# Optimization experiments

Measured on AMD Instinct MI355X. Metric: run time of the kernel, lower is better.

The kernel has to match this reference:

```python
import jax, jax.numpy as jnp
import numpy as np

N_NODES = 50000
N_EDGES = 800000
IN_DIM = 256
HID_DIM = 256
OUT_DIM = 2


def setup_inputs() -> dict:
    key = jax.random.key(0)
    ks = jax.random.split(key, 8)
    x = jax.random.normal(ks[0], (N_NODES, IN_DIM), dtype=jnp.float32)
    edge_index = jax.random.randint(ks[1], (2, N_EDGES), 0, N_NODES, dtype=jnp.int64)
    # GCNConv weights (PyG: out = norm_agg(x @ W) + b), Glorot-ish scale
    W1 = jax.random.normal(ks[2], (IN_DIM, HID_DIM), dtype=jnp.float32) / np.sqrt(IN_DIM)
    b1 = jnp.zeros((HID_DIM,), dtype=jnp.float32)
    W2 = jax.random.normal(ks[3], (HID_DIM, HID_DIM), dtype=jnp.float32) / np.sqrt(HID_DIM)
    b2 = jnp.zeros((HID_DIM,), dtype=jnp.float32)
    Wfc = jax.random.normal(ks[4], (HID_DIM, OUT_DIM), dtype=jnp.float32) / np.sqrt(HID_DIM)
    bfc = jnp.zeros((OUT_DIM,), dtype=jnp.float32)
    return {"x": x, "edge_index": edge_index, "W1": W1, "b1": b1,
            "W2": W2, "b2": b2, "Wfc": Wfc, "bfc": bfc}


def _edge_norm(edge_index, n_nodes):
    # GCNConv: add self-loops, symmetric normalization D^-1/2 A_hat D^-1/2
    loop = jnp.arange(n_nodes, dtype=edge_index.dtype)
    src = jnp.concatenate([edge_index[0], loop])  # [E+N]
    dst = jnp.concatenate([edge_index[1], loop])  # [E+N]
    deg = jax.ops.segment_sum(jnp.ones_like(dst, dtype=jnp.float32), dst,
                              num_segments=n_nodes)
    dis = jnp.where(deg > 0, jax.lax.rsqrt(deg), 0.0)  # deg_inv_sqrt [N]
    norm = dis[src] * dis[dst]  # [E+N]
    return src, dst, norm


def _gcn_layer(x, W, b, src, dst, norm, n_nodes):
    h = x @ W  # [N, F_out]
    msg = h[src] * norm[:, None]  # gather + scale, [E+N, F_out]
    return jax.ops.segment_sum(msg, dst, num_segments=n_nodes) + b


def reference(x, edge_index, W1, b1, W2, b2, Wfc, bfc):
    n = x.shape[0]
    src, dst, norm = _edge_norm(edge_index, n)
    h = jax.nn.relu(_gcn_layer(x, W1, b1, src, dst, norm, n))
    # dropout is identity in eval mode
    h = jax.nn.relu(_gcn_layer(h, W2, b2, src, dst, norm, n))
    logits = h @ Wfc + bfc
    return jax.nn.log_softmax(logits, axis=1)
```

## Files before the change

### kernel.cpp

```cpp
#include <hip/hip_runtime.h>
#include <math.h>

#define N_NODES 50000
#define N_EDGES 800000
#define DIM 256
#define SCAN_BLOCKS ((N_NODES + 255) / 256)
#define NXBLK 12500
#define NDEGBLK ((N_EDGES + 255) / 256)

typedef short bf16x8 __attribute__((ext_vector_type(8)));
typedef float f32x4 __attribute__((ext_vector_type(4)));

__device__ __forceinline__ float bf2f(unsigned short u) {
    return __uint_as_float(((unsigned)u) << 16);
}
__device__ __forceinline__ unsigned short f2bf(float f) {
    unsigned u = __float_as_uint(f);
    return (unsigned short)((u + 0x7fffu + ((u >> 16) & 1u)) >> 16);
}

__global__ __launch_bounds__(256) void k_prep(const float* __restrict__ x,
                                              unsigned short* __restrict__ xb,
                                              const float* __restrict__ W1,
                                              unsigned short* __restrict__ W1t,
                                              const float* __restrict__ W2,
                                              unsigned short* __restrict__ W2t,
                                              const int* __restrict__ dst,
                                              int* __restrict__ ideg) {
    int bid = blockIdx.x;
    int tid = threadIdx.x;
    if (bid < NXBLK) {
        int i = bid * 256 + tid;
        float4 v = ((const float4*)x)[i];
        ((ushort4*)xb)[i] = make_ushort4(f2bf(v.x), f2bf(v.y), f2bf(v.z), f2bf(v.w));
    } else if (bid < NXBLK + 256) {
        int n = bid - NXBLK;
        W1t[n * 256 + tid] = f2bf(W1[tid * 256 + n]);
    } else if (bid < NXBLK + 512) {
        int n = bid - NXBLK - 256;
        W2t[n * 256 + tid] = f2bf(W2[tid * 256 + n]);
    } else {
        int e = (bid - NXBLK - 512) * 256 + tid;
        if (e < N_EDGES) atomicAdd(&ideg[dst[e]], 1);
    }
}


__global__ __launch_bounds__(256) void k_scan_block(const int* __restrict__ ideg,
                                                    int* __restrict__ rowptr,
                                                    int* __restrict__ blocksum) {
    __shared__ int s[256];
    int t = threadIdx.x;
    int i = blockIdx.x * 256 + t;
    int v = (i < N_NODES) ? ideg[i] : 0;
    s[t] = v;
    for (int off = 1; off < 256; off <<= 1) {
        __syncthreads();
        int add = (t >= off) ? s[t - off] : 0;
        __syncthreads();
        s[t] += add;
    }
    __syncthreads();
    if (i < N_NODES) rowptr[i] = s[t] - v;
    if (t == 255) blocksum[blockIdx.x] = s[255];
}

__global__ __launch_bounds__(256) void k_scan_add(int* __restrict__ rowptr,
                                                  const int* __restrict__ blocksum,
                                                  int* __restrict__ cursor,
                                                  const int* __restrict__ ideg,
                                                  float* __restrict__ dis) {
    __shared__ int s[256];
    int t = threadIdx.x;
    int v = (t < SCAN_BLOCKS) ? blocksum[t] : 0;
    s[t] = v;
    for (int off = 1; off < 256; off <<= 1) {
        __syncthreads();
        int add = (t >= off) ? s[t - off] : 0;
        __syncthreads();
        s[t] += add;
    }
    __syncthreads();
    int excl = s[t] - v;
    __syncthreads();
    s[t] = excl;
    __syncthreads();
    int off = s[blockIdx.x];

    int i = blockIdx.x * 256 + t;
    if (i < N_NODES) {
        int r = rowptr[i] + off;
        rowptr[i] = r;
        cursor[i] = r;
        dis[i] = rsqrtf((float)(ideg[i] + 1));
    }
    if (i == 0) rowptr[N_NODES] = N_EDGES;
}

__global__ void k_csr_fill(const int* __restrict__ src, const int* __restrict__ dst,
                           int* __restrict__ cursor, int* __restrict__ csr_src) {
    int e = blockIdx.x * blockDim.x + threadIdx.x;
    if (e < N_EDGES) {
        int pos = atomicAdd(&cursor[dst[e]], 1);
        csr_src[pos] = src[e];
    }
}

__global__ __launch_bounds__(256) void k_agg_bf16(const unsigned short* __restrict__ in,
                                                  const float* __restrict__ dis,
                                                  const int* __restrict__ rowptr,
                                                  const int* __restrict__ csr_src,
                                                  unsigned short* __restrict__ out) {
    int node = blockIdx.x * 4 + (threadIdx.x >> 6);
    if (node >= N_NODES) return;
    int lane = threadIdx.x & 63;
    int f = lane * 4;

    float dn = dis[node];
    ushort4 sv = *(const ushort4*)(in + (size_t)node * DIM + f);
    float a0 = dn * bf2f(sv.x);
    float a1 = dn * bf2f(sv.y);
    float a2 = dn * bf2f(sv.z);
    float a3 = dn * bf2f(sv.w);

    int e = rowptr[node];
    int eEnd = rowptr[node + 1];
    for (; e + 3 < eEnd; e += 4) {
        int s0 = csr_src[e], s1 = csr_src[e + 1], s2 = csr_src[e + 2], s3 = csr_src[e + 3];
        float w0 = dis[s0], w1 = dis[s1], w2 = dis[s2], w3 = dis[s3];
        ushort4 v0 = *(const ushort4*)(in + (size_t)s0 * DIM + f);
        ushort4 v1 = *(const ushort4*)(in + (size_t)s1 * DIM + f);
        ushort4 v2 = *(const ushort4*)(in + (size_t)s2 * DIM + f);
        ushort4 v3 = *(const ushort4*)(in + (size_t)s3 * DIM + f);
        a0 += w0 * bf2f(v0.x) + w1 * bf2f(v1.x) + w2 * bf2f(v2.x) + w3 * bf2f(v3.x);
        a1 += w0 * bf2f(v0.y) + w1 * bf2f(v1.y) + w2 * bf2f(v2.y) + w3 * bf2f(v3.y);
        a2 += w0 * bf2f(v0.z) + w1 * bf2f(v1.z) + w2 * bf2f(v2.z) + w3 * bf2f(v3.z);
        a3 += w0 * bf2f(v0.w) + w1 * bf2f(v1.w) + w2 * bf2f(v2.w) + w3 * bf2f(v3.w);
    }
    for (; e < eEnd; ++e) {
        int s0 = csr_src[e];
        float w0 = dis[s0];
        ushort4 v0 = *(const ushort4*)(in + (size_t)s0 * DIM + f);
        a0 += w0 * bf2f(v0.x);
        a1 += w0 * bf2f(v0.y);
        a2 += w0 * bf2f(v0.z);
        a3 += w0 * bf2f(v0.w);
    }
    a0 *= dn; a1 *= dn; a2 *= dn; a3 *= dn;
    *(ushort4*)(out + (size_t)node * DIM + f) =
        make_ushort4(f2bf(a0), f2bf(a1), f2bf(a2), f2bf(a3));
}

__global__ __launch_bounds__(256) void k_gemm_wide(const unsigned short* __restrict__ A,
                                                   const unsigned short* __restrict__ Wt,
                                                   const float* __restrict__ bias,
                                                   unsigned short* __restrict__ C, int M) {
    __shared__ unsigned short As[4][128][8];
    __shared__ unsigned short Bs[4][256][8];

    int tid = threadIdx.x;
    int lane = tid & 63;
    int wave = tid >> 6;
    int lr = lane & 15;
    int lc = lane >> 4;

    int rowBase = blockIdx.x * 128;

    f32x4 acc[2][16] = {};

    int r = tid >> 2;
    int c = tid & 3;

    for (int k0 = 0; k0 < DIM; k0 += 32) {
        float4 z = make_float4(0.f, 0.f, 0.f, 0.f);
        int gr0 = rowBase + r;
        int gr1 = rowBase + r + 64;
        float4 va0 = (gr0 < M) ? *(const float4*)(A + (size_t)gr0 * DIM + k0 + c * 8) : z;
        float4 va1 = (gr1 < M) ? *(const float4*)(A + (size_t)gr1 * DIM + k0 + c * 8) : z;
        *(float4*)&As[c][r][0]      = va0;
        *(float4*)&As[c][r + 64][0] = va1;
#pragma unroll
        for (int j = 0; j < 4; ++j) {
            int brow = r + 64 * j;
            *(float4*)&Bs[c][brow][0] = *(const float4*)(Wt + (size_t)brow * DIM + k0 + c * 8);
        }
        __syncthreads();

        bf16x8 af[2];
#pragma unroll
        for (int m = 0; m < 2; ++m)
            af[m] = *(const bf16x8*)&As[lc][wave * 32 + m * 16 + lr][0];
#pragma unroll
        for (int n = 0; n < 16; ++n) {
            bf16x8 bfr = *(const bf16x8*)&Bs[lc][n * 16 + lr][0];
            acc[0][n] = __builtin_amdgcn_mfma_f32_16x16x32_bf16(af[0], bfr, acc[0][n], 0, 0, 0);
            acc[1][n] = __builtin_amdgcn_mfma_f32_16x16x32_bf16(af[1], bfr, acc[1][n], 0, 0, 0);
        }
        __syncthreads();
    }

    float bv[16];
#pragma unroll
    for (int n = 0; n < 16; ++n) bv[n] = bias[n * 16 + lr];

#pragma unroll
    for (int m = 0; m < 2; ++m) {
#pragma unroll
        for (int reg = 0; reg < 4; ++reg) {
            int row = rowBase + wave * 32 + m * 16 + lc * 4 + reg;
            if (row < M) {
#pragma unroll
                for (int n = 0; n < 16; ++n) {
                    float v = fmaxf(acc[m][n][reg] + bv[n], 0.f);
                    C[(size_t)row * DIM + n * 16 + lr] = f2bf(v);
                }
            }
        }
    }
}

__global__ __launch_bounds__(256) void k_gemm_fc(const unsigned short* __restrict__ A,
                                                 const unsigned short* __restrict__ Wt,
                                                 const float* __restrict__ bias,
                                                 const float* __restrict__ Wfc,
                                                 const float* __restrict__ bfc,
                                                 float* __restrict__ out, int M) {
    __shared__ unsigned short As[4][128][8];
    __shared__ unsigned short Bs[4][256][8];

    int tid = threadIdx.x;
    int lane = tid & 63;
    int wave = tid >> 6;
    int lr = lane & 15;
    int lc = lane >> 4;

    int rowBase = blockIdx.x * 128;

    f32x4 acc[2][16] = {};

    int r = tid >> 2;
    int c = tid & 3;

    for (int k0 = 0; k0 < DIM; k0 += 32) {
        float4 z = make_float4(0.f, 0.f, 0.f, 0.f);
        int gr0 = rowBase + r;
        int gr1 = rowBase + r + 64;
        float4 va0 = (gr0 < M) ? *(const float4*)(A + (size_t)gr0 * DIM + k0 + c * 8) : z;
        float4 va1 = (gr1 < M) ? *(const float4*)(A + (size_t)gr1 * DIM + k0 + c * 8) : z;
        *(float4*)&As[c][r][0]      = va0;
        *(float4*)&As[c][r + 64][0] = va1;
#pragma unroll
        for (int j = 0; j < 4; ++j) {
            int brow = r + 64 * j;
            *(float4*)&Bs[c][brow][0] = *(const float4*)(Wt + (size_t)brow * DIM + k0 + c * 8);
        }
        __syncthreads();

        bf16x8 af[2];
#pragma unroll
        for (int m = 0; m < 2; ++m)
            af[m] = *(const bf16x8*)&As[lc][wave * 32 + m * 16 + lr][0];
#pragma unroll
        for (int n = 0; n < 16; ++n) {
            bf16x8 bfr = *(const bf16x8*)&Bs[lc][n * 16 + lr][0];
            acc[0][n] = __builtin_amdgcn_mfma_f32_16x16x32_bf16(af[0], bfr, acc[0][n], 0, 0, 0);
            acc[1][n] = __builtin_amdgcn_mfma_f32_16x16x32_bf16(af[1], bfr, acc[1][n], 0, 0, 0);
        }
        __syncthreads();
    }

    float bv[16], wf0[16], wf1[16];
#pragma unroll
    for (int n = 0; n < 16; ++n) {
        int col = n * 16 + lr;
        bv[n]  = bias[col];
        wf0[n] = Wfc[col * 2 + 0];
        wf1[n] = Wfc[col * 2 + 1];
    }
    float bb0 = bfc[0], bb1 = bfc[1];

#pragma unroll
    for (int m = 0; m < 2; ++m) {
#pragma unroll
        for (int reg = 0; reg < 4; ++reg) {
            int row = rowBase + wave * 32 + m * 16 + lc * 4 + reg;
            float s0 = 0.f, s1 = 0.f;
#pragma unroll
            for (int n = 0; n < 16; ++n) {
                float v = fmaxf(acc[m][n][reg] + bv[n], 0.f);
                s0 += v * wf0[n];
                s1 += v * wf1[n];
            }
#pragma unroll
            for (int o = 1; o < 16; o <<= 1) {
                s0 += __shfl_xor(s0, o);
                s1 += __shfl_xor(s1, o);
            }
            if (lr == 0 && row < M) {
                float l0 = s0 + bb0;
                float l1 = s1 + bb1;
                float mx = fmaxf(l0, l1);
                float lse = mx + logf(expf(l0 - mx) + expf(l1 - mx));
                out[(size_t)row * 2 + 0] = l0 - lse;
                out[(size_t)row * 2 + 1] = l1 - lse;
            }
        }
    }
}

extern "C" void kernel_launch(void* const* d_in, const int* in_sizes, int n_in,
                              void* d_out, int out_size, void* d_ws, size_t ws_size,
                              hipStream_t stream) {
    const float* x      = (const float*)d_in[0];
    const int* ei       = (const int*)d_in[1];
    const int* esrc     = ei;
    const int* edst     = ei + N_EDGES;
    const float* W1  = (const float*)d_in[2];
    const float* b1  = (const float*)d_in[3];
    const float* W2  = (const float*)d_in[4];
    const float* b2  = (const float*)d_in[5];
    const float* Wfc = (const float*)d_in[6];
    const float* bfc = (const float*)d_in[7];
    float* out = (float*)d_out;

    const size_t NF = (size_t)N_NODES * DIM;
    unsigned short* P0 = (unsigned short*)d_ws;
    unsigned short* P1 = P0 + NF;
    unsigned short* P2 = P1 + NF;
    unsigned short* W1t = P2 + NF;
    unsigned short* W2t = W1t + 256 * 256;
    float* dis    = (float*)(W2t + 256 * 256);
    int* ideg     = (int*)(dis + N_NODES);
    int* rowptr   = ideg + N_NODES;
    int* cursor   = rowptr + N_NODES + 1;
    int* blocksum = cursor + N_NODES;
    int* csr_src  = blocksum + 256;

    hipMemsetAsync(ideg, 0, N_NODES * sizeof(int), stream);
    k_prep<<<NXBLK + 512 + NDEGBLK, 256, 0, stream>>>(x, P0, W1, W1t, W2, W2t, edst, ideg);
    k_scan_block<<<SCAN_BLOCKS, 256, 0, stream>>>(ideg, rowptr, blocksum);
    k_scan_add<<<SCAN_BLOCKS, 256, 0, stream>>>(rowptr, blocksum, cursor, ideg, dis);
    k_csr_fill<<<(N_EDGES + 255) / 256, 256, 0, stream>>>(esrc, edst, cursor, csr_src);

    int aggBlocks = (N_NODES + 3) / 4;
    int gemmBlocks = (N_NODES + 127) / 128;

    k_agg_bf16<<<aggBlocks, 256, 0, stream>>>(P0, dis, rowptr, csr_src, P1);
    k_gemm_wide<<<gemmBlocks, 256, 0, stream>>>(P1, W1t, b1, P2, N_NODES);

    k_agg_bf16<<<aggBlocks, 256, 0, stream>>>(P2, dis, rowptr, csr_src, P0);
    k_gemm_fc<<<gemmBlocks, 256, 0, stream>>>(P0, W2t, b2, Wfc, bfc, out, N_NODES);
}
```

Before: 290.4 us.

## Fuse sparse aggregation into GEMM blocks via swizzled LDS tile

Merges each layer's CSR neighbour aggregation with the following dense GEMM. A 512-thread block first aggregates 128 node rows straight into a swizzled shared-memory A tile, then runs the MFMA GEMM from that tile with a 4x2 wave layout over N. This removes the intermediate aggregated-feature buffer and its global write/read round trip, and drops two kernel launches. The cost is fewer, larger blocks (391) that each handle 16 nodes per wave, which lowers parallelism for the latency-bound gather phase and leaves the matrix cores idle while it runs. In the FC variant the two column halves reduce through shared memory.

```diff
diff --git a/kernel.cpp b/kernel.cpp
--- a/kernel.cpp
+++ b/kernel.cpp
@@ -7,6 +7,8 @@
 #define SCAN_BLOCKS ((N_NODES + 255) / 256)
 #define NXBLK 12500
 #define NDEGBLK ((N_EDGES + 255) / 256)
+#define ROWS 128
+#define GBLK ((N_NODES + ROWS - 1) / ROWS)
 
 typedef short bf16x8 __attribute__((ext_vector_type(8)));
 typedef float f32x4 __attribute__((ext_vector_type(4)));
@@ -106,203 +108,157 @@
     }
 }
 
-__global__ __launch_bounds__(256) void k_agg_bf16(const unsigned short* __restrict__ in,
-                                                  const float* __restrict__ dis,
-                                                  const int* __restrict__ rowptr,
-                                                  const int* __restrict__ csr_src,
-                                                  unsigned short* __restrict__ out) {
-    int node = blockIdx.x * 4 + (threadIdx.x >> 6);
-    if (node >= N_NODES) return;
-    int lane = threadIdx.x & 63;
-    int f = lane * 4;
-
-    float dn = dis[node];
-    ushort4 sv = *(const ushort4*)(in + (size_t)node * DIM + f);
-    float a0 = dn * bf2f(sv.x);
-    float a1 = dn * bf2f(sv.y);
-    float a2 = dn * bf2f(sv.z);
-    float a3 = dn * bf2f(sv.w);
-
-    int e = rowptr[node];
-    int eEnd = rowptr[node + 1];
-    for (; e + 3 < eEnd; e += 4) {
-        int s0 = csr_src[e], s1 = csr_src[e + 1], s2 = csr_src[e + 2], s3 = csr_src[e + 3];
-        float w0 = dis[s0], w1 = dis[s1], w2 = dis[s2], w3 = dis[s3];
-        ushort4 v0 = *(const ushort4*)(in + (size_t)s0 * DIM + f);
-        ushort4 v1 = *(const ushort4*)(in + (size_t)s1 * DIM + f);
-        ushort4 v2 = *(const ushort4*)(in + (size_t)s2 * DIM + f);
-        ushort4 v3 = *(const ushort4*)(in + (size_t)s3 * DIM + f);
-        a0 += w0 * bf2f(v0.x) + w1 * bf2f(v1.x) + w2 * bf2f(v2.x) + w3 * bf2f(v3.x);
-        a1 += w0 * bf2f(v0.y) + w1 * bf2f(v1.y) + w2 * bf2f(v2.y) + w3 * bf2f(v3.y);
-        a2 += w0 * bf2f(v0.z) + w1 * bf2f(v1.z) + w2 * bf2f(v2.z) + w3 * bf2f(v3.z);
-        a3 += w0 * bf2f(v0.w) + w1 * bf2f(v1.w) + w2 * bf2f(v2.w) + w3 * bf2f(v3.w);
-    }
-    for (; e < eEnd; ++e) {
-        int s0 = csr_src[e];
-        float w0 = dis[s0];
-        ushort4 v0 = *(const ushort4*)(in + (size_t)s0 * DIM + f);
-        a0 += w0 * bf2f(v0.x);
-        a1 += w0 * bf2f(v0.y);
-        a2 += w0 * bf2f(v0.z);
-        a3 += w0 * bf2f(v0.w);
-    }
-    a0 *= dn; a1 *= dn; a2 *= dn; a3 *= dn;
-    *(ushort4*)(out + (size_t)node * DIM + f) =
-        make_ushort4(f2bf(a0), f2bf(a1), f2bf(a2), f2bf(a3));
-}
-
-__global__ __launch_bounds__(256) void k_gemm_wide(const unsigned short* __restrict__ A,
-                                                   const unsigned short* __restrict__ Wt,
-                                                   const float* __restrict__ bias,
-                                                   unsigned short* __restrict__ C, int M) {
-    __shared__ unsigned short As[4][128][8];
+template <int FC>
+__global__ __launch_bounds__(512) void k_fused(const unsigned short* __restrict__ in,
+                                               const float* __restrict__ dis,
+                                               const int* __restrict__ rowptr,
+                                               const int* __restrict__ csr_src,
+                                               const unsigned short* __restrict__ Wt,
+                                               const float* __restrict__ bias,
+                                               const float* __restrict__ Wfc,
+                                               const float* __restrict__ bfc,
+                                               unsigned short* __restrict__ outB,
+                                               float* __restrict__ outF) {
+    __shared__ unsigned short As[ROWS * DIM];
     __shared__ unsigned short Bs[4][256][8];
 
     int tid = threadIdx.x;
     int lane = tid & 63;
     int wave = tid >> 6;
+    int rowBase = blockIdx.x * ROWS;
+
+    for (int i = 0; i < 16; ++i) {
+        int rl = wave * 16 + i;
+        int node = rowBase + rl;
+        float a0 = 0.f, a1 = 0.f, a2 = 0.f, a3 = 0.f;
+        if (node < N_NODES) {
+            int f = lane * 4;
+            float dn = dis[node];
+            ushort4 sv = *(const ushort4*)(in + (size_t)node * DIM + f);
+            a0 = dn * bf2f(sv.x);
+            a1 = dn * bf2f(sv.y);
+            a2 = dn * bf2f(sv.z);
+            a3 = dn * bf2f(sv.w);
+            int e = rowptr[node];
+            int eEnd = rowptr[node + 1];
+            for (; e + 3 < eEnd; e += 4) {
+                int s0 = csr_src[e], s1 = csr_src[e + 1], s2 = csr_src[e + 2], s3 = csr_src[e + 3];
+                float w0 = dis[s0], w1 = dis[s1], w2 = dis[s2], w3 = dis[s3];
+                ushort4 v0 = *(const ushort4*)(in + (size_t)s0 * DIM + f);
+                ushort4 v1 = *(const ushort4*)(in + (size_t)s1 * DIM + f);
+                ushort4 v2 = *(const ushort4*)(in + (size_t)s2 * DIM + f);
+                ushort4 v3 = *(const ushort4*)(in + (size_t)s3 * DIM + f);
+                a0 += w0 * bf2f(v0.x) + w1 * bf2f(v1.x) + w2 * bf2f(v2.x) + w3 * bf2f(v3.x);
+                a1 += w0 * bf2f(v0.y) + w1 * bf2f(v1.y) + w2 * bf2f(v2.y) + w3 * bf2f(v3.y);
+                a2 += w0 * bf2f(v0.z) + w1 * bf2f(v1.z) + w2 * bf2f(v2.z) + w3 * bf2f(v3.z);
+                a3 += w0 * bf2f(v0.w) + w1 * bf2f(v1.w) + w2 * bf2f(v2.w) + w3 * bf2f(v3.w);
+            }
+            for (; e < eEnd; ++e) {
+                int s0 = csr_src[e];
+                float w0 = dis[s0];
+                ushort4 v0 = *(const ushort4*)(in + (size_t)s0 * DIM + f);
+                a0 += w0 * bf2f(v0.x);
+                a1 += w0 * bf2f(v0.y);
+                a2 += w0 * bf2f(v0.z);
+                a3 += w0 * bf2f(v0.w);
+            }
+            a0 *= dn; a1 *= dn; a2 *= dn; a3 *= dn;
+        }
+        unsigned off = (unsigned)rl * 512u + (((unsigned)lane * 8u) ^ (((unsigned)rl & 15u) << 4));
+        *(ushort4*)((char*)As + off) = make_ushort4(f2bf(a0), f2bf(a1), f2bf(a2), f2bf(a3));
+    }
+    __syncthreads();
+
+    int wm = wave >> 1;
+    int wn = wave & 1;
     int lr = lane & 15;
     int lc = lane >> 4;
 
-    int rowBase = blockIdx.x * 128;
-
-    f32x4 acc[2][16] = {};
-
-    int r = tid >> 2;
-    int c = tid & 3;
+    f32x4 acc[2][8] = {};
+
+    int brow = tid >> 1;
+    int cc = (tid & 1) * 2;
 
     for (int k0 = 0; k0 < DIM; k0 += 32) {
-        float4 z = make_float4(0.f, 0.f, 0.f, 0.f);
-        int gr0 = rowBase + r;
-        int gr1 = rowBase + r + 64;
-        float4 va0 = (gr0 < M) ? *(const float4*)(A + (size_t)gr0 * DIM + k0 + c * 8) : z;
-        float4 va1 = (gr1 < M) ? *(const float4*)(A + (size_t)gr1 * DIM + k0 + c * 8) : z;
-        *(float4*)&As[c][r][0]      = va0;
-        *(float4*)&As[c][r + 64][0] = va1;
-#pragma unroll
-        for (int j = 0; j < 4; ++j) {
-            int brow = r + 64 * j;
-            *(float4*)&Bs[c][brow][0] = *(const float4*)(Wt + (size_t)brow * DIM + k0 + c * 8);
-        }
-        __syncthreads();
-
-        bf16x8 af[2];
-#pragma unroll
-        for (int m = 0; m < 2; ++m)
-            af[m] = *(const bf16x8*)&As[lc][wave * 32 + m * 16 + lr][0];
-#pragma unroll
-        for (int n = 0; n < 16; ++n) {
-            bf16x8 bfr = *(const bf16x8*)&Bs[lc][n * 16 + lr][0];
-            acc[0][n] = __builtin_amdgcn_mfma_f32_16x16x32_bf16(af[0], bfr, acc[0][n], 0, 0, 0);
-            acc[1][n] = __builtin_amdgcn_mfma_f32_16x16x32_bf16(af[1], bfr, acc[1][n], 0, 0, 0);
-        }
-        __syncthreads();
-    }
-
-    float bv[16];
-#pragma unroll
-    for (int n = 0; n < 16; ++n) bv[n] = bias[n * 16 + lr];
-
-#pragma unroll
-    for (int m = 0; m < 2; ++m) {
-#pragma unroll
-        for (int reg = 0; reg < 4; ++reg) {
-            int row = rowBase + wave * 32 + m * 16 + lc * 4 + reg;
-            if (row < M) {
-#pragma unroll
-                for (int n = 0; n < 16; ++n) {
+        *(float4*)&Bs[cc][brow][0]     = *(const float4*)(Wt + (size_t)brow * DIM + k0 + cc * 8);
+        *(float4*)&Bs[cc + 1][brow][0] = *(const float4*)(Wt + (size_t)brow * DIM + k0 + cc * 8 + 8);
+        __syncthreads();
+
+        int r0 = wm * 32 + lr;
+        int r1 = r0 + 16;
+        unsigned cb = (unsigned)(k0 * 2 + lc * 16);
+        bf16x8 af0 = *(const bf16x8*)((const char*)As + (unsigned)r0 * 512u + (cb ^ (((unsigned)r0 & 15u) << 4)));
+        bf16x8 af1 = *(const bf16x8*)((const char*)As + (unsigned)r1 * 512u + (cb ^ (((unsigned)r1 & 15u) << 4)));
+#pragma unroll
+        for (int n = 0; n < 8; ++n) {
+            bf16x8 bfr = *(const bf16x8*)&Bs[lc][wn * 128 + n * 16 + lr][0];
+            acc[0][n] = __builtin_amdgcn_mfma_f32_16x16x32_bf16(af0, bfr, acc[0][n], 0, 0, 0);
+            acc[1][n] = __builtin_amdgcn_mfma_f32_16x16x32_bf16(af1, bfr, acc[1][n], 0, 0, 0);
+        }
+        __syncthreads();
+    }
+
+    if (FC) {
+        float bv[8], wf0[8], wf1[8];
+#pragma unroll
+        for (int n = 0; n < 8; ++n) {
+            int col = wn * 128 + n * 16 + lr;
+            bv[n]  = bias[col];
+            wf0[n] = Wfc[col * 2 + 0];
+            wf1[n] = Wfc[col * 2 + 1];
+        }
+        float* part = (float*)&Bs[0][0][0];
+#pragma unroll
+        for (int m = 0; m < 2; ++m) {
+#pragma unroll
+            for (int reg = 0; reg < 4; ++reg) {
+                int rl = wm * 32 + m * 16 + lc * 4 + reg;
+                float s0 = 0.f, s1 = 0.f;
+#pragma unroll
+                for (int n = 0; n < 8; ++n) {
                     float v = fmaxf(acc[m][n][reg] + bv[n], 0.f);
-                    C[(size_t)row * DIM + n * 16 + lr] = f2bf(v);
+                    s0 += v * wf0[n];
+                    s1 += v * wf1[n];
                 }
-            }
-        }
-    }
-}
-
-__global__ __launch_bounds__(256) void k_gemm_fc(const unsigned short* __restrict__ A,
-                                                 const unsigned short* __restrict__ Wt,
-                                                 const float* __restrict__ bias,
-                                                 const float* __restrict__ Wfc,
-                                                 const float* __restrict__ bfc,
-                                                 float* __restrict__ out, int M) {
-    __shared__ unsigned short As[4][128][8];
-    __shared__ unsigned short Bs[4][256][8];
-
-    int tid = threadIdx.x;
-    int lane = tid & 63;
-    int wave = tid >> 6;
-    int lr = lane & 15;
-    int lc = lane >> 4;
-
-    int rowBase = blockIdx.x * 128;
-
-    f32x4 acc[2][16] = {};
-
-    int r = tid >> 2;
-    int c = tid & 3;
-
-    for (int k0 = 0; k0 < DIM; k0 += 32) {
-        float4 z = make_float4(0.f, 0.f, 0.f, 0.f);
-        int gr0 = rowBase + r;
-        int gr1 = rowBase + r + 64;
-        float4 va0 = (gr0 < M) ? *(const float4*)(A + (size_t)gr0 * DIM + k0 + c * 8) : z;
-        float4 va1 = (gr1 < M) ? *(const float4*)(A + (size_t)gr1 * DIM + k0 + c * 8) : z;
-        *(float4*)&As[c][r][0]      = va0;
-        *(float4*)&As[c][r + 64][0] = va1;
-#pragma unroll
-        for (int j = 0; j < 4; ++j) {
-            int brow = r + 64 * j;
-            *(float4*)&Bs[c][brow][0] = *(const float4*)(Wt + (size_t)brow * DIM + k0 + c * 8);
-        }
-        __syncthreads();
-
-        bf16x8 af[2];
-#pragma unroll
-        for (int m = 0; m < 2; ++m)
-            af[m] = *(const bf16x8*)&As[lc][wave * 32 + m * 16 + lr][0];
-#pragma unroll
-        for (int n = 0; n < 16; ++n) {
-            bf16x8 bfr = *(const bf16x8*)&Bs[lc][n * 16 + lr][0];
-            acc[0][n] = __builtin_amdgcn_mfma_f32_16x16x32_bf16(af[0], bfr, acc[0][n], 0, 0, 0);
-            acc[1][n] = __builtin_amdgcn_mfma_f32_16x16x32_bf16(af[1], bfr, acc[1][n], 0, 0, 0);
-        }
-        __syncthreads();
-    }
-
-    float bv[16], wf0[16], wf1[16];
-#pragma unroll
-    for (int n = 0; n < 16; ++n) {
-        int col = n * 16 + lr;
-        bv[n]  = bias[col];
-        wf0[n] = Wfc[col * 2 + 0];
-        wf1[n] = Wfc[col * 2 + 1];
-    }
-    float bb0 = bfc[0], bb1 = bfc[1];
-
-#pragma unroll
-    for (int m = 0; m < 2; ++m) {
-#pragma unroll
-        for (int reg = 0; reg < 4; ++reg) {
-            int row = rowBase + wave * 32 + m * 16 + lc * 4 + reg;
-            float s0 = 0.f, s1 = 0.f;
-#pragma unroll
-            for (int n = 0; n < 16; ++n) {
-                float v = fmaxf(acc[m][n][reg] + bv[n], 0.f);
-                s0 += v * wf0[n];
-                s1 += v * wf1[n];
-            }
-#pragma unroll
-            for (int o = 1; o < 16; o <<= 1) {
-                s0 += __shfl_xor(s0, o);
-                s1 += __shfl_xor(s1, o);
-            }
-            if (lr == 0 && row < M) {
-                float l0 = s0 + bb0;
-                float l1 = s1 + bb1;
+#pragma unroll
+                for (int o = 1; o < 16; o <<= 1) {
+                    s0 += __shfl_xor(s0, o);
+                    s1 += __shfl_xor(s1, o);
+                }
+                if (lr == 0) {
+                    part[rl * 4 + wn * 2 + 0] = s0;
+                    part[rl * 4 + wn * 2 + 1] = s1;
+                }
+            }
+        }
+        __syncthreads();
+        if (tid < ROWS) {
+            int row = rowBase + tid;
+            if (row < N_NODES) {
+                float l0 = part[tid * 4 + 0] + part[tid * 4 + 2] + bfc[0];
+                float l1 = part[tid * 4 + 1] + part[tid * 4 + 3] + bfc[1];
                 float mx = fmaxf(l0, l1);
                 float lse = mx + logf(expf(l0 - mx) + expf(l1 - mx));
-                out[(size_t)row * 2 + 0] = l0 - lse;
-                out[(size_t)row * 2 + 1] = l1 - lse;
+                outF[(size_t)row * 2 + 0] = l0 - lse;
+                outF[(size_t)row * 2 + 1] = l1 - lse;
+            }
+        }
+    } else {
+        float bv[8];
+#pragma unroll
+        for (int n = 0; n < 8; ++n) bv[n] = bias[wn * 128 + n * 16 + lr];
+#pragma unroll
+        for (int m = 0; m < 2; ++m) {
+#pragma unroll
+            for (int reg = 0; reg < 4; ++reg) {
+                int row = rowBase + wm * 32 + m * 16 + lc * 4 + reg;
+                if (row < N_NODES) {
+#pragma unroll
+                    for (int n = 0; n < 8; ++n) {
+                        float v = fmaxf(acc[m][n][reg] + bv[n], 0.f);
+                        outB[(size_t)row * DIM + wn * 128 + n * 16 + lr] = f2bf(v);
+                    }
+                }
             }
         }
     }
@@ -326,8 +282,7 @@
     const size_t NF = (size_t)N_NODES * DIM;
     unsigned short* P0 = (unsigned short*)d_ws;
     unsigned short* P1 = P0 + NF;
-    unsigned short* P2 = P1 + NF;
-    unsigned short* W1t = P2 + NF;
+    unsigned short* W1t = P1 + NF;
     unsigned short* W2t = W1t + 256 * 256;
     float* dis    = (float*)(W2t + 256 * 256);
     int* ideg     = (int*)(dis + N_NODES);
@@ -342,12 +297,10 @@
     k_scan_add<<<SCAN_BLOCKS, 256, 0, stream>>>(rowptr, blocksum, cursor, ideg, dis);
     k_csr_fill<<<(N_EDGES + 255) / 256, 256, 0, stream>>>(esrc, edst, cursor, csr_src);
 
-    int aggBlocks = (N_NODES + 3) / 4;
-    int gemmBlocks = (N_NODES + 127) / 128;
-
-    k_agg_bf16<<<aggBlocks, 256, 0, stream>>>(P0, dis, rowptr, csr_src, P1);
-    k_gemm_wide<<<gemmBlocks, 256, 0, stream>>>(P1, W1t, b1, P2, N_NODES);
-
-    k_agg_bf16<<<aggBlocks, 256, 0, stream>>>(P2, dis, rowptr, csr_src, P0);
-    k_gemm_fc<<<gemmBlocks, 256, 0, stream>>>(P0, W2t, b2, Wfc, bfc, out, N_NODES);
-}
+    k_fused<0><<<GBLK, 512, 0, stream>>>(P0, dis, rowptr, csr_src, W1t, b1,
+                                         (const float*)nullptr, (const float*)nullptr,
+                                         P1, (float*)nullptr);
+    k_fused<1><<<GBLK, 512, 0, stream>>>(P1, dis, rowptr, csr_src, W2t, b2,
+                                         Wfc, bfc,
+                                         (unsigned short*)nullptr, out);
+}
```

After: 391.0 us. +34.7%, slower.

## Split aggregation into feature strips with per-edge precomputed weights

Applied to the files above, without the earlier changes.

The aggregation kernel is restructured so each block handles one 32-feature strip for a contiguous chunk of nodes. Each wave processes 8 edges in parallel and reduces them with cross-lane shuffles. The goal is L2 locality, since blocks with the same strip share a narrower working set, and more memory-level parallelism per wave. The CSR fill now stores each edge's source dis weight, which removes a dependent gather in the inner loop. In exchange, csr_src is re-read for every strip and there are fixed chunk sizes with possible imbalance and shuffle overhead.

```diff
diff --git a/kernel.cpp b/kernel.cpp
--- a/kernel.cpp
+++ b/kernel.cpp
@@ -7,6 +7,9 @@
 #define SCAN_BLOCKS ((N_NODES + 255) / 256)
 #define NXBLK 12500
 #define NDEGBLK ((N_EDGES + 255) / 256)
+#define NSTRIP 8
+#define NCHUNK 256
+#define CHUNKSZ ((N_NODES + NCHUNK - 1) / NCHUNK)
 
 typedef short bf16x8 __attribute__((ext_vector_type(8)));
 typedef float f32x4 __attribute__((ext_vector_type(4)));
@@ -98,57 +101,67 @@
 }
 
 __global__ void k_csr_fill(const int* __restrict__ src, const int* __restrict__ dst,
-                           int* __restrict__ cursor, int* __restrict__ csr_src) {
+                           int* __restrict__ cursor, int* __restrict__ csr_src,
+                           float* __restrict__ csr_w, const float* __restrict__ dis) {
     int e = blockIdx.x * blockDim.x + threadIdx.x;
     if (e < N_EDGES) {
+        int s = src[e];
         int pos = atomicAdd(&cursor[dst[e]], 1);
-        csr_src[pos] = src[e];
-    }
-}
-
-__global__ __launch_bounds__(256) void k_agg_bf16(const unsigned short* __restrict__ in,
-                                                  const float* __restrict__ dis,
-                                                  const int* __restrict__ rowptr,
-                                                  const int* __restrict__ csr_src,
-                                                  unsigned short* __restrict__ out) {
-    int node = blockIdx.x * 4 + (threadIdx.x >> 6);
-    if (node >= N_NODES) return;
+        csr_src[pos] = s;
+        csr_w[pos] = dis[s];
+    }
+}
+
+__global__ __launch_bounds__(256) void k_agg_strip(const unsigned short* __restrict__ in,
+                                                   const float* __restrict__ dis,
+                                                   const int* __restrict__ rowptr,
+                                                   const int* __restrict__ csr_src,
+                                                   const float* __restrict__ csr_w,
+                                                   unsigned short* __restrict__ out) {
+    int strip = blockIdx.x & (NSTRIP - 1);
+    int chunk = blockIdx.x >> 3;
+    int wave = threadIdx.x >> 6;
     int lane = threadIdx.x & 63;
-    int f = lane * 4;
-
-    float dn = dis[node];
-    ushort4 sv = *(const ushort4*)(in + (size_t)node * DIM + f);
-    float a0 = dn * bf2f(sv.x);
-    float a1 = dn * bf2f(sv.y);
-    float a2 = dn * bf2f(sv.z);
-    float a3 = dn * bf2f(sv.w);
-
-    int e = rowptr[node];
-    int eEnd = rowptr[node + 1];
-    for (; e + 3 < eEnd; e += 4) {
-        int s0 = csr_src[e], s1 = csr_src[e + 1], s2 = csr_src[e + 2], s3 = csr_src[e + 3];
-        float w0 = dis[s0], w1 = dis[s1], w2 = dis[s2], w3 = dis[s3];
-        ushort4 v0 = *(const ushort4*)(in + (size_t)s0 * DIM + f);
-        ushort4 v1 = *(const ushort4*)(in + (size_t)s1 * DIM + f);
-        ushort4 v2 = *(const ushort4*)(in + (size_t)s2 * DIM + f);
-        ushort4 v3 = *(const ushort4*)(in + (size_t)s3 * DIM + f);
-        a0 += w0 * bf2f(v0.x) + w1 * bf2f(v1.x) + w2 * bf2f(v2.x) + w3 * bf2f(v3.x);
-        a1 += w0 * bf2f(v0.y) + w1 * bf2f(v1.y) + w2 * bf2f(v2.y) + w3 * bf2f(v3.y);
-        a2 += w0 * bf2f(v0.z) + w1 * bf2f(v1.z) + w2 * bf2f(v2.z) + w3 * bf2f(v3.z);
-        a3 += w0 * bf2f(v0.w) + w1 * bf2f(v1.w) + w2 * bf2f(v2.w) + w3 * bf2f(v3.w);
-    }
-    for (; e < eEnd; ++e) {
-        int s0 = csr_src[e];
-        float w0 = dis[s0];
-        ushort4 v0 = *(const ushort4*)(in + (size_t)s0 * DIM + f);
-        a0 += w0 * bf2f(v0.x);
-        a1 += w0 * bf2f(v0.y);
-        a2 += w0 * bf2f(v0.z);
-        a3 += w0 * bf2f(v0.w);
-    }
-    a0 *= dn; a1 *= dn; a2 *= dn; a3 *= dn;
-    *(ushort4*)(out + (size_t)node * DIM + f) =
-        make_ushort4(f2bf(a0), f2bf(a1), f2bf(a2), f2bf(a3));
+    int j = lane >> 3;
+    int d = lane & 7;
+    int f = strip * 32 + d * 4;
+
+    int nodeEnd = min((chunk + 1) * CHUNKSZ, N_NODES);
+    for (int node = chunk * CHUNKSZ + wave; node < nodeEnd; node += 4) {
+        float dn = dis[node];
+        float a0 = 0.f, a1 = 0.f, a2 = 0.f, a3 = 0.f;
+        if (j == 0) {
+            ushort4 v = *(const ushort4*)(in + (size_t)node * DIM + f);
+            a0 = dn * bf2f(v.x); a1 = dn * bf2f(v.y);
+            a2 = dn * bf2f(v.z); a3 = dn * bf2f(v.w);
+        }
+        int e0 = rowptr[node];
+        int e1 = rowptr[node + 1];
+        for (int e = e0; e < e1; e += 8) {
+            int ee = e + j;
+            bool valid = ee < e1;
+            int s = valid ? __builtin_nontemporal_load(&csr_src[ee]) : 0;
+            float w = valid ? __builtin_nontemporal_load(&csr_w[ee]) : 0.f;
+            ushort4 v = *(const ushort4*)(in + (size_t)s * DIM + f);
+            a0 += w * bf2f(v.x);
+            a1 += w * bf2f(v.y);
+            a2 += w * bf2f(v.z);
+            a3 += w * bf2f(v.w);
+        }
+#pragma unroll
+        for (int o = 8; o < 64; o <<= 1) {
+            a0 += __shfl_xor(a0, o);
+            a1 += __shfl_xor(a1, o);
+            a2 += __shfl_xor(a2, o);
+            a3 += __shfl_xor(a3, o);
+        }
+        if (j == 0) {
+            unsigned lo = (unsigned)f2bf(dn * a0) | ((unsigned)f2bf(dn * a1) << 16);
+            unsigned hi = (unsigned)f2bf(dn * a2) | ((unsigned)f2bf(dn * a3) << 16);
+            unsigned long long pk = (unsigned long long)lo | ((unsigned long long)hi << 32);
+            __builtin_nontemporal_store(pk, (unsigned long long*)(out + (size_t)node * DIM + f));
+        }
+    }
 }
 
 __global__ __launch_bounds__(256) void k_gemm_wide(const unsigned short* __restrict__ A,
@@ -180,8 +193,8 @@
         *(float4*)&As[c][r][0]      = va0;
         *(float4*)&As[c][r + 64][0] = va1;
 #pragma unroll
-        for (int j = 0; j < 4; ++j) {
-            int brow = r + 64 * j;
+        for (int jj = 0; jj < 4; ++jj) {
+            int brow = r + 64 * jj;
             *(float4*)&Bs[c][brow][0] = *(const float4*)(Wt + (size_t)brow * DIM + k0 + c * 8);
         }
         __syncthreads();
@@ -250,8 +263,8 @@
         *(float4*)&As[c][r][0]      = va0;
         *(float4*)&As[c][r + 64][0] = va1;
 #pragma unroll
-        for (int j = 0; j < 4; ++j) {
-            int brow = r + 64 * j;
+        for (int jj = 0; jj < 4; ++jj) {
+            int brow = r + 64 * jj;
             *(float4*)&Bs[c][brow][0] = *(const float4*)(Wt + (size_t)brow * DIM + k0 + c * 8);
         }
         __syncthreads();
@@ -335,19 +348,20 @@
     int* cursor   = rowptr + N_NODES + 1;
     int* blocksum = cursor + N_NODES;
     int* csr_src  = blocksum + 256;
-
-    hipMemsetAsync(ideg, 0, N_NODES * sizeof(int), stream);
+    float* csr_w  = (float*)(csr_src + N_EDGES);
+
+    (void)hipMemsetAsync(ideg, 0, N_NODES * sizeof(int), stream);
     k_prep<<<NXBLK + 512 + NDEGBLK, 256, 0, stream>>>(x, P0, W1, W1t, W2, W2t, edst, ideg);
     k_scan_block<<<SCAN_BLOCKS, 256, 0, stream>>>(ideg, rowptr, blocksum);
     k_scan_add<<<SCAN_BLOCKS, 256, 0, stream>>>(rowptr, blocksum, cursor, ideg, dis);
-    k_csr_fill<<<(N_EDGES + 255) / 256, 256, 0, stream>>>(esrc, edst, cursor, csr_src);
-
-    int aggBlocks = (N_NODES + 3) / 4;
+    k_csr_fill<<<(N_EDGES + 255) / 256, 256, 0, stream>>>(esrc, edst, cursor, csr_src, csr_w, dis);
+
+    int aggBlocks = NCHUNK * NSTRIP;
     int gemmBlocks = (N_NODES + 127) / 128;
 
-    k_agg_bf16<<<aggBlocks, 256, 0, stream>>>(P0, dis, rowptr, csr_src, P1);
+    k_agg_strip<<<aggBlocks, 256, 0, stream>>>(P0, dis, rowptr, csr_src, csr_w, P1);
     k_gemm_wide<<<gemmBlocks, 256, 0, stream>>>(P1, W1t, b1, P2, N_NODES);
 
-    k_agg_bf16<<<aggBlocks, 256, 0, stream>>>(P2, dis, rowptr, csr_src, P0);
+    k_agg_strip<<<aggBlocks, 256, 0, stream>>>(P2, dis, rowptr, csr_src, csr_w, P0);
     k_gemm_fc<<<gemmBlocks, 256, 0, stream>>>(P0, W2t, b2, Wfc, bfc, out, N_NODES);
 }
```

Result: slower. 606.8 us (+108.9%).
